# Kernel tuning notes

Hardware: AMD Instinct MI355X
Metric: run time of the kernel (lower is better)

The kernel has to match this reference:

```python
import jax, jax.numpy as jnp
import numpy as np

NOISE = 0.02
P_CONST = 1.0
NUM_LAYERS = 7


def setup_inputs() -> dict:
    key = jax.random.key(0)
    k1, k2, k3, k4 = jax.random.split(key, 4)
    B, Nt, K, L = 2048, 64, 40, NUM_LAYERS
    sqrtP = np.sqrt(P_CONST)
    return {
        'H_real': jax.random.normal(k1, (B, Nt, K), dtype=jnp.float32),
        'H_imag': jax.random.normal(k2, (B, Nt, K), dtype=jnp.float32),
        'eta': jnp.ones((L,), dtype=jnp.float32) * (0.1 / sqrtP),
        'U': jax.random.normal(k3, (L, Nt, Nt), dtype=jnp.float32) * (0.01 / sqrtP),
        'b': jax.random.normal(k4, (L, Nt, K), dtype=jnp.float32) * (0.01 / sqrtP),
    }


def _rate_total(Wr, Wi, Hc):
    # sum over batch of (sum_k log2(1+sinr_k) - power_penalty)
    W = Wr + 1j * Wi                                   # [B,Nt,K] complex
    HW = jnp.einsum('bnk,bnl->bkl', jnp.conj(Hc), W)   # [B,K,K]
    pw = jnp.abs(HW) ** 2                              # |h_k^H w_l|^2
    desired = jnp.diagonal(pw, axis1=1, axis2=2)       # [B,K]
    interference = pw.sum(axis=2) - desired
    sinr = desired / (interference + NOISE)
    rates = jnp.log2(1.0 + sinr).sum()
    power = jnp.sum(Wr * Wr + Wi * Wi, axis=(1, 2))    # ||W||_F^2 per batch
    penalty = jnp.mean((power - P_CONST) ** 2) * 0.01
    B = Wr.shape[0]
    return rates - B * penalty


def reference(H_real, H_imag, eta, U, b):
    Hc = H_real + 1j * H_imag
    B, Nt, K = H_real.shape
    Wr = jnp.zeros((B, Nt, K), dtype=jnp.float32)
    Wi = jnp.zeros((B, Nt, K), dtype=jnp.float32)
    grad_fn = jax.grad(_rate_total, argnums=(0, 1))
    for t in range(NUM_LAYERS):
        g_r, g_i = grad_fn(Wr, Wi, Hc)                 # torch grad: dL/dx + i dL/dy
        Ug_r = jnp.einsum('nm,bmk->bnk', U[t], g_r)
        Ug_i = jnp.einsum('nm,bmk->bnk', U[t], g_i)
        step_r = Ug_r - Ug_i
        step_i = Ug_i + Ug_r
        Wr = Wr - eta[t] * step_r + b[t]
        Wi = Wi - eta[t] * step_i
    # final power normalization
    norm = jnp.sqrt(jnp.sum(Wr * Wr + Wi * Wi, axis=(1, 2), keepdims=True))
    scale = jnp.sqrt(P_CONST) / (norm + 1e-6)
    Wr = Wr * scale
    Wi = Wi * scale
    return Wr + 1j * Wi
```

## Files before the change

kernel.cpp:

```cpp
#include <hip/hip_runtime.h>
#include <math.h>

typedef _Float16 h16;
typedef __attribute__((ext_vector_type(2))) _Float16 h16x2;
typedef __attribute__((ext_vector_type(4))) _Float16 h16x4;
typedef __attribute__((ext_vector_type(8))) _Float16 h16x8;
typedef __attribute__((ext_vector_type(4))) float f32x4;

#define NBATCH 2048
#define NT 64
#define KK 40
#define NL 7
#define SIGMA 0.02f
#define INVLN2 1.4426950408889634f

#define RA   0
#define RB   (40*128)
#define HCK  (2*40*128)
#define UOF  (3*40*128)
#define LDSH (UOF + 64*64)

#define SWZ(row, c)  ((c) ^ (((row)&7)<<3))
#define SWZW(row, c) ((c) ^ (((row)&15)<<3))
#define MFMA16(a,b,c) __builtin_amdgcn_mfma_f32_16x16x32_f16((a),(b),(c),0,0,0)

static __device__ __forceinline__ float DOT2(h16x2 a, h16x2 b, float c) {
#if __has_builtin(__builtin_amdgcn_fdot2)
    return __builtin_amdgcn_fdot2(a, b, c, false);
#else
    return fmaf((float)a.x, (float)b.x, fmaf((float)a.y, (float)b.y, c));
#endif
}
static __device__ __forceinline__ h16x2 PK(float x, float y) {
    h16x2 r; r.x = (h16)x; r.y = (h16)y; return r;
}
static __device__ __forceinline__ h16x8 conjA(h16x8 v) {
    union { h16x8 h; unsigned u[4]; } x; x.h = v;
    #pragma unroll
    for (int i=0;i<4;++i){ unsigned t=x.u[i]; t=(t>>16)|(t<<16); x.u[i]=t^0x80000000u; }
    return x.h;
}
static __device__ __forceinline__ h16x8 imB(h16x8 v) {
    union { h16x8 h; unsigned u[4]; } x; x.h = v;
    #pragma unroll
    for (int i=0;i<4;++i){ unsigned t=x.u[i]; t=(t>>16)|(t<<16); x.u[i]=t^0x00008000u; }
    return x.h;
}
static __device__ __forceinline__ h16x8 zsel(h16x8 v, bool p) {
    union { h16x8 h; unsigned u[4]; } x; x.h = v;
    #pragma unroll
    for (int i=0;i<4;++i) x.u[i] = p ? x.u[i] : 0u;
    return x.h;
}

__global__ __launch_bounds__(256, 2) void gpnet_kernel(
    const float* __restrict__ gHr, const float* __restrict__ gHi,
    const float* __restrict__ gEta, const float* __restrict__ gU,
    const float* __restrict__ gB, float* __restrict__ gOut, int outFloats)
{
    __shared__ __align__(16) h16 sh[LDSH];
    __shared__ float sRed[4];

    const int tid = threadIdx.x;
    const int wv  = tid >> 6;
    const int ln  = tid & 63;
    const int col = ln & 15;
    const int g   = ln >> 4;

    const int bb = blockIdx.x;
    const float* hr = gHr + (size_t)bb * NT * KK;
    const float* hi = gHi + (size_t)bb * NT * KK;

    for (int i = tid; i < NT*KK; i += 256) {
        int n = i / KK, k = i % KK;
        *(h16x2*)(sh + HCK + k*128 + SWZW(k, 2*n)) = PK(hr[i], hi[i]);
        *(h16x2*)(sh + RA  + k*128 + SWZW(k, 2*n)) = PK(gB[i], 0.f);
    }
    float Wr[3][4], Wi[3][4];
    float ps = 0.f;
    #pragma unroll
    for (int ct = 0; ct < 3; ++ct)
        #pragma unroll
        for (int r = 0; r < 4; ++r) {
            int n = 16*wv + 4*g + r, l = col + 16*ct;
            float b0 = (l < KK) ? gB[n*KK + l] : 0.f;
            Wr[ct][r] = b0; Wi[ct][r] = 0.f;
            ps += b0 * b0;
        }
    #pragma unroll
    for (int off = 32; off; off >>= 1) ps += __shfl_down(ps, off, 64);
    if (ln == 0) sRed[wv] = ps;
    __syncthreads();

    for (int t = 1; t < NL; ++t) {
        const int P = (t & 1) ? RA : RB;
        const int Q = (t & 1) ? RB : RA;
        const int GREo = P, GIMo = P + 40*64;

        const float pw   = sRed[0] + sRed[1] + sRed[2] + sRed[3];
        const float cpen = 0.04f * (pw - 1.0f);
        const float etat = gEta[t];

        if (wv < 3) {
            const int kcol = col + 16*wv;
            const bool vK = (kcol < KK);
            const int kC = vK ? kcol : 0;
            #pragma unroll
            for (int rt = 0; rt < 3; ++rt) {
                f32x4 aRe = (f32x4){0.f,0.f,0.f,0.f};
                f32x4 aIm = (f32x4){0.f,0.f,0.f,0.f};
                const int lrow = col + 16*rt;
                const int lC = (lrow < KK) ? lrow : 0;
                #pragma unroll
                for (int q = 0; q < 4; ++q) {
                    h16x8 bf = *(const h16x8*)(sh + HCK + kC*128 + SWZW(kC, g*8 + 32*q));
                    bf = zsel(bf, vK);
                    h16x8 af = *(const h16x8*)(sh + P + lC*128 + SWZW(lC, g*8 + 32*q));
                    aRe = MFMA16(af, bf, aRe);
                    aIm = MFMA16(conjA(af), bf, aIm);
                }
                #pragma unroll
                for (int r = 0; r < 4; ++r) {
                    int l = 16*rt + 4*g + r;
                    if (l < KK)
                        *(h16x2*)(sh + Q + l*128 + SWZ(l, 2*kcol)) = PK(aRe[r], aIm[r]);
                }
            }
        } else {
            const float2* u2 = (const float2*)(gU + (size_t)t * NT * NT);
            #pragma unroll 8
            for (int j = 0; j < 32; ++j) {
                int e2 = j*64 + ln;
                float2 v = u2[e2];
                int n = e2 >> 5, m2 = (e2 & 31) * 2;
                *(h16x2*)(sh + UOF + n*64 + SWZ(n, m2)) = PK(v.x, v.y);
            }
        }
        __syncthreads();

        if (tid < 160) {
            const int k = tid >> 2, q = tid & 3;
            h16x2 va[10];
            #pragma unroll
            for (int ii = 0; ii < 10; ++ii)
                va[ii] = *(const h16x2*)(sh + Q + (q*10+ii)*128 + SWZ(q*10+ii, 2*k));
            float rs = 0.f, dd = 0.f;
            #pragma unroll
            for (int ii = 0; ii < 10; ++ii) rs = DOT2(va[ii], va[ii], rs);
            const int dk = k - q*10;
            if (dk >= 0 && dk < 10) dd = DOT2(va[dk], va[dk], 0.f);
            rs += __shfl_xor(rs, 1, 64); rs += __shfl_xor(rs, 2, 64);
            dd += __shfl_xor(dd, 1, 64); dd += __shfl_xor(dd, 2, 64);
            float T  = rs + SIGMA, Is = rs - dd + SIGMA;
            float cA_ = 2.f * INVLN2 / T;
            float cC_ = -2.f * INVLN2 * dd / (Is * T);
            #pragma unroll
            for (int ii = 0; ii < 10; ++ii) {
                int l = q*10 + ii;
                float c = (l == k) ? cA_ : cC_;
                *(h16x2*)(sh + Q + l*128 + SWZ(l, 2*k)) =
                    PK((float)va[ii].x * c, -(float)va[ii].y * c);
            }
        }
        __syncthreads();

        {
            const int nrow = col + 16*wv;
            const int n0w = 16*wv + 4*g;
            #pragma unroll
            for (int ct = 0; ct < 3; ++ct) {
                f32x4 gRe = (f32x4){0.f,0.f,0.f,0.f};
                f32x4 gIm = (f32x4){0.f,0.f,0.f,0.f};
                const int lr = col + 16*ct;
                const int lrC = (lr < KK) ? lr : 0;
                #pragma unroll
                for (int q = 0; q < 3; ++q) {
                    h16x8 af;
                    #pragma unroll
                    for (int j = 0; j < 8; ++j) af[j] = (h16)0.f;
                    if (q < 2 || g < 2) {
                        const int kb = g*4 + 16*q;
                        #pragma unroll
                        for (int i = 0; i < 4; ++i) {
                            h16x2 p = *(const h16x2*)(sh + HCK + (kb+i)*128 + SWZW(kb+i, 2*nrow));
                            af[2*i] = p.x; af[2*i+1] = p.y;
                        }
                    }
                    h16x8 bf = *(const h16x8*)(sh + Q + lrC*128 + SWZ(lrC, g*8 + 32*q));
                    gRe = MFMA16(af, bf, gRe);
                    gIm = MFMA16(af, imB(bf), gIm);
                }
                if (lr < KK) {
                    h16x4 g4, q4;
                    #pragma unroll
                    for (int r = 0; r < 4; ++r) {
                        g4[r] = (h16)(gRe[r] - cpen * Wr[ct][r]);
                        q4[r] = (h16)(gIm[r] - cpen * Wi[ct][r]);
                    }
                    *(h16x4*)(sh + GREo + lr*64 + SWZ(lr, n0w)) = g4;
                    *(h16x4*)(sh + GIMo + lr*64 + SWZ(lr, n0w)) = q4;
                }
            }
        }
        __syncthreads();

        float ps2 = 0.f;
        {
            const int nrow = col + 16*wv;
            const int n0w = 16*wv + 4*g;
            const float* bt = gB + (size_t)t*NT*KK;
            #pragma unroll
            for (int ct = 0; ct < 3; ++ct) {
                f32x4 cRe = (f32x4){0.f,0.f,0.f,0.f};
                f32x4 cIm = (f32x4){0.f,0.f,0.f,0.f};
                const int l = col + 16*ct;
                const int lC = (l < KK) ? l : 0;
                #pragma unroll
                for (int q = 0; q < 2; ++q) {
                    h16x8 af = *(const h16x8*)(sh + UOF + nrow*64 + SWZ(nrow, g*8 + 32*q));
                    h16x8 fre = *(const h16x8*)(sh + GREo + lC*64 + SWZ(lC, g*8 + 32*q));
                    h16x8 fim = *(const h16x8*)(sh + GIMo + lC*64 + SWZ(lC, g*8 + 32*q));
                    cRe = MFMA16(af, fre, cRe);
                    cIm = MFMA16(af, fim, cIm);
                }
                h16x8 wvv;
                #pragma unroll
                for (int r = 0; r < 4; ++r) {
                    int n = n0w + r;
                    float br = (l < KK) ? bt[n*KK + l] : 0.f;
                    float ur = cRe[r], ui = cIm[r];
                    float wr = Wr[ct][r] - etat*(ur - ui) + br;
                    float wi = Wi[ct][r] - etat*(ui + ur);
                    Wr[ct][r] = wr; Wi[ct][r] = wi;
                    wvv[2*r]   = (h16)wr;
                    wvv[2*r+1] = (h16)wi;
                    if (l < KK) ps2 += wr*wr + wi*wi;
                }
                if (t < NL-1 && l < KK)
                    *(h16x8*)(sh + Q + l*128 + SWZW(l, 2*n0w)) = wvv;
            }
        }
        #pragma unroll
        for (int off = 32; off; off >>= 1) ps2 += __shfl_down(ps2, off, 64);
        if (ln == 0) sRed[wv] = ps2;
        __syncthreads();
    }

    const float pwf   = sRed[0] + sRed[1] + sRed[2] + sRed[3];
    const float scale = 1.0f / (sqrtf(pwf) + 1e-6f);

    if (outFloats >= 2 * NBATCH * NT * KK) {
        float2* ob = (float2*)(gOut + (size_t)bb * NT * KK * 2);
        #pragma unroll
        for (int ct = 0; ct < 3; ++ct)
            #pragma unroll
            for (int r = 0; r < 4; ++r) {
                int n = 16*wv + 4*g + r, l = col + 16*ct;
                if (l < KK) {
                    float2 v; v.x = Wr[ct][r]*scale; v.y = Wi[ct][r]*scale;
                    ob[n*KK + l] = v;
                }
            }
    } else {
        float* ob = gOut + (size_t)bb * NT * KK;
        #pragma unroll
        for (int ct = 0; ct < 3; ++ct)
            #pragma unroll
            for (int r = 0; r < 4; ++r) {
                int n = 16*wv + 4*g + r, l = col + 16*ct;
                if (l < KK) ob[n*KK + l] = Wr[ct][r] * scale;
            }
    }
}

extern "C" void kernel_launch(void* const* d_in, const int* in_sizes, int n_in,
                              void* d_out, int out_size, void* d_ws, size_t ws_size,
                              hipStream_t stream) {
    (void)in_sizes; (void)n_in; (void)d_ws; (void)ws_size;
    const float* Hr  = (const float*)d_in[0];
    const float* Hi  = (const float*)d_in[1];
    const float* eta = (const float*)d_in[2];
    const float* U   = (const float*)d_in[3];
    const float* b   = (const float*)d_in[4];
    float* out = (float*)d_out;
    gpnet_kernel<<<NBATCH, 256, 0, stream>>>(Hr, Hi, eta, U, b, out, out_size);
}
```

Measured before the change: 122.9 us.

## Process one batch item per wavefront, keeping W in registers without block syncs

Each wavefront now handles a whole batch item, with four items per block, in its own LDS region. This replaces the four-wave cooperative split and removes the __syncthreads barriers in favour of wave-local compiler fences. W is held in registers as packed fp16 MFMA operands rather than fp32 and written back to LDS. U is now read straight from global memory into registers instead of being staged in LDS. The risks are lower parallelism per item (2048 waves total), higher register pressure, and fp16 storage of W between layers, which costs accuracy.

```diff
diff --git a/kernel.cpp b/kernel.cpp
--- a/kernel.cpp
+++ b/kernel.cpp
@@ -14,15 +14,17 @@
 #define SIGMA 0.02f
 #define INVLN2 1.4426950408889634f
 
-#define RA   0
-#define RB   (40*128)
-#define HCK  (2*40*128)
-#define UOF  (3*40*128)
-#define LDSH (UOF + 64*64)
+#define ITEMSZ 15360
+#define SOFF   0
+#define GREOFF 5120
+#define GIMOFF 7680
+#define HCKOFF 10240
+#define LDSH   (4*ITEMSZ)
 
 #define SWZ(row, c)  ((c) ^ (((row)&7)<<3))
 #define SWZW(row, c) ((c) ^ (((row)&15)<<3))
 #define MFMA16(a,b,c) __builtin_amdgcn_mfma_f32_16x16x32_f16((a),(b),(c),0,0,0)
+#define CFENCE() asm volatile("" ::: "memory")
 
 static __device__ __forceinline__ float DOT2(h16x2 a, h16x2 b, float c) {
 #if __has_builtin(__builtin_amdgcn_fdot2)
@@ -52,223 +54,252 @@
     for (int i=0;i<4;++i) x.u[i] = p ? x.u[i] : 0u;
     return x.h;
 }
-
-__global__ __launch_bounds__(256, 2) void gpnet_kernel(
+static __device__ __forceinline__ h16x8 zero8() {
+    h16x8 v;
+    #pragma unroll
+    for (int j=0;j<8;++j) v[j] = (h16)0.f;
+    return v;
+}
+
+__global__ __launch_bounds__(256) void gpnet_kernel(
     const float* __restrict__ gHr, const float* __restrict__ gHi,
     const float* __restrict__ gEta, const float* __restrict__ gU,
     const float* __restrict__ gB, float* __restrict__ gOut, int outFloats)
 {
     __shared__ __align__(16) h16 sh[LDSH];
-    __shared__ float sRed[4];
 
     const int tid = threadIdx.x;
     const int wv  = tid >> 6;
     const int ln  = tid & 63;
     const int col = ln & 15;
     const int g   = ln >> 4;
-
-    const int bb = blockIdx.x;
+    const int IB  = wv * ITEMSZ;
+
+    const int bb = blockIdx.x * 4 + wv;
     const float* hr = gHr + (size_t)bb * NT * KK;
     const float* hi = gHi + (size_t)bb * NT * KK;
 
-    for (int i = tid; i < NT*KK; i += 256) {
+    for (int j = 0; j < 40; ++j) {
+        int i = j*64 + ln;
         int n = i / KK, k = i % KK;
-        *(h16x2*)(sh + HCK + k*128 + SWZW(k, 2*n)) = PK(hr[i], hi[i]);
-        *(h16x2*)(sh + RA  + k*128 + SWZW(k, 2*n)) = PK(gB[i], 0.f);
+        *(h16x2*)(sh + IB + HCKOFF + k*128 + SWZW(k, 2*n)) = PK(hr[i], hi[i]);
     }
-    float Wr[3][4], Wi[3][4];
+    h16x8 Wh[4][3];
     float ps = 0.f;
     #pragma unroll
-    for (int ct = 0; ct < 3; ++ct)
-        #pragma unroll
-        for (int r = 0; r < 4; ++r) {
-            int n = 16*wv + 4*g + r, l = col + 16*ct;
-            float b0 = (l < KK) ? gB[n*KK + l] : 0.f;
-            Wr[ct][r] = b0; Wi[ct][r] = 0.f;
-            ps += b0 * b0;
+    for (int nb = 0; nb < 4; ++nb)
+        #pragma unroll
+        for (int lt = 0; lt < 3; ++lt) {
+            int l = col + 16*lt;
+            h16x8 v = zero8();
+            if (l < KK) {
+                #pragma unroll
+                for (int r = 0; r < 4; ++r) {
+                    int n = 16*nb + 4*g + r;
+                    float b0 = gB[n*KK + l];
+                    v[2*r] = (h16)b0;
+                    ps += b0 * b0;
+                }
+            }
+            Wh[nb][lt] = v;
         }
     #pragma unroll
     for (int off = 32; off; off >>= 1) ps += __shfl_down(ps, off, 64);
-    if (ln == 0) sRed[wv] = ps;
-    __syncthreads();
-
+    float pw = __shfl(ps, 0, 64);
+    CFENCE();
+
+    #pragma unroll 1
     for (int t = 1; t < NL; ++t) {
-        const int P = (t & 1) ? RA : RB;
-        const int Q = (t & 1) ? RB : RA;
-        const int GREo = P, GIMo = P + 40*64;
-
-        const float pw   = sRed[0] + sRed[1] + sRed[2] + sRed[3];
         const float cpen = 0.04f * (pw - 1.0f);
         const float etat = gEta[t];
 
-        if (wv < 3) {
-            const int kcol = col + 16*wv;
+        #pragma unroll
+        for (int kc = 0; kc < 3; ++kc) {
+            const int kcol = col + 16*kc;
             const bool vK = (kcol < KK);
             const int kC = vK ? kcol : 0;
+            h16x8 bf[4];
+            #pragma unroll
+            for (int q = 0; q < 4; ++q) {
+                bf[q] = *(const h16x8*)(sh + IB + HCKOFF + kC*128 + SWZW(kC, g*8 + 32*q));
+                bf[q] = zsel(bf[q], vK);
+            }
             #pragma unroll
             for (int rt = 0; rt < 3; ++rt) {
                 f32x4 aRe = (f32x4){0.f,0.f,0.f,0.f};
                 f32x4 aIm = (f32x4){0.f,0.f,0.f,0.f};
-                const int lrow = col + 16*rt;
-                const int lC = (lrow < KK) ? lrow : 0;
                 #pragma unroll
                 for (int q = 0; q < 4; ++q) {
-                    h16x8 bf = *(const h16x8*)(sh + HCK + kC*128 + SWZW(kC, g*8 + 32*q));
-                    bf = zsel(bf, vK);
-                    h16x8 af = *(const h16x8*)(sh + P + lC*128 + SWZW(lC, g*8 + 32*q));
-                    aRe = MFMA16(af, bf, aRe);
-                    aIm = MFMA16(conjA(af), bf, aIm);
+                    h16x8 af = Wh[q][rt];
+                    aRe = MFMA16(af, bf[q], aRe);
+                    aIm = MFMA16(conjA(af), bf[q], aIm);
                 }
                 #pragma unroll
                 for (int r = 0; r < 4; ++r) {
                     int l = 16*rt + 4*g + r;
                     if (l < KK)
-                        *(h16x2*)(sh + Q + l*128 + SWZ(l, 2*kcol)) = PK(aRe[r], aIm[r]);
-                }
-            }
-        } else {
-            const float2* u2 = (const float2*)(gU + (size_t)t * NT * NT);
-            #pragma unroll 8
-            for (int j = 0; j < 32; ++j) {
-                int e2 = j*64 + ln;
-                float2 v = u2[e2];
-                int n = e2 >> 5, m2 = (e2 & 31) * 2;
-                *(h16x2*)(sh + UOF + n*64 + SWZ(n, m2)) = PK(v.x, v.y);
-            }
-        }
-        __syncthreads();
-
-        if (tid < 160) {
-            const int k = tid >> 2, q = tid & 3;
-            h16x2 va[10];
-            #pragma unroll
-            for (int ii = 0; ii < 10; ++ii)
-                va[ii] = *(const h16x2*)(sh + Q + (q*10+ii)*128 + SWZ(q*10+ii, 2*k));
+                        *(h16x2*)(sh + IB + SOFF + l*128 + SWZ(l, 2*kcol)) =
+                            PK(aRe[r], aIm[r]);
+                }
+            }
+        }
+        CFENCE();
+
+        if (ln < KK) {
+            const int k = ln;
             float rs = 0.f, dd = 0.f;
             #pragma unroll
-            for (int ii = 0; ii < 10; ++ii) rs = DOT2(va[ii], va[ii], rs);
-            const int dk = k - q*10;
-            if (dk >= 0 && dk < 10) dd = DOT2(va[dk], va[dk], 0.f);
-            rs += __shfl_xor(rs, 1, 64); rs += __shfl_xor(rs, 2, 64);
-            dd += __shfl_xor(dd, 1, 64); dd += __shfl_xor(dd, 2, 64);
+            for (int l = 0; l < KK; ++l) {
+                h16x2 v = *(const h16x2*)(sh + IB + SOFF + l*128 + SWZ(l, 2*k));
+                float p2 = DOT2(v, v, 0.f);
+                rs += p2;
+                if (l == k) dd = p2;
+            }
             float T  = rs + SIGMA, Is = rs - dd + SIGMA;
             float cA_ = 2.f * INVLN2 / T;
             float cC_ = -2.f * INVLN2 * dd / (Is * T);
             #pragma unroll
-            for (int ii = 0; ii < 10; ++ii) {
-                int l = q*10 + ii;
+            for (int l = 0; l < KK; ++l) {
+                h16x2 v = *(const h16x2*)(sh + IB + SOFF + l*128 + SWZ(l, 2*k));
                 float c = (l == k) ? cA_ : cC_;
-                *(h16x2*)(sh + Q + l*128 + SWZ(l, 2*k)) =
-                    PK((float)va[ii].x * c, -(float)va[ii].y * c);
-            }
-        }
-        __syncthreads();
-
-        {
-            const int nrow = col + 16*wv;
-            const int n0w = 16*wv + 4*g;
-            #pragma unroll
-            for (int ct = 0; ct < 3; ++ct) {
+                *(h16x2*)(sh + IB + SOFF + l*128 + SWZ(l, 2*k)) =
+                    PK((float)v.x * c, -(float)v.y * c);
+            }
+        }
+        CFENCE();
+
+        #pragma unroll
+        for (int nb = 0; nb < 4; ++nb) {
+            const int nrow = col + 16*nb;
+            h16x8 afh[3];
+            #pragma unroll
+            for (int q = 0; q < 3; ++q) {
+                h16x8 v = zero8();
+                if (q < 2 || g < 2) {
+                    const int kb = g*4 + 16*q;
+                    #pragma unroll
+                    for (int i = 0; i < 4; ++i) {
+                        h16x2 p = *(const h16x2*)(sh + IB + HCKOFF + (kb+i)*128 + SWZW(kb+i, 2*nrow));
+                        v[2*i] = p.x; v[2*i+1] = p.y;
+                    }
+                }
+                afh[q] = v;
+            }
+            #pragma unroll
+            for (int lt = 0; lt < 3; ++lt) {
+                const int lr = col + 16*lt;
+                const int lrC = (lr < KK) ? lr : 0;
                 f32x4 gRe = (f32x4){0.f,0.f,0.f,0.f};
                 f32x4 gIm = (f32x4){0.f,0.f,0.f,0.f};
-                const int lr = col + 16*ct;
-                const int lrC = (lr < KK) ? lr : 0;
                 #pragma unroll
                 for (int q = 0; q < 3; ++q) {
-                    h16x8 af;
-                    #pragma unroll
-                    for (int j = 0; j < 8; ++j) af[j] = (h16)0.f;
-                    if (q < 2 || g < 2) {
-                        const int kb = g*4 + 16*q;
-                        #pragma unroll
-                        for (int i = 0; i < 4; ++i) {
-                            h16x2 p = *(const h16x2*)(sh + HCK + (kb+i)*128 + SWZW(kb+i, 2*nrow));
-                            af[2*i] = p.x; af[2*i+1] = p.y;
-                        }
-                    }
-                    h16x8 bf = *(const h16x8*)(sh + Q + lrC*128 + SWZ(lrC, g*8 + 32*q));
-                    gRe = MFMA16(af, bf, gRe);
-                    gIm = MFMA16(af, imB(bf), gIm);
+                    h16x8 bf = *(const h16x8*)(sh + IB + SOFF + lrC*128 + SWZ(lrC, g*8 + 32*q));
+                    gRe = MFMA16(afh[q], bf, gRe);
+                    gIm = MFMA16(afh[q], imB(bf), gIm);
                 }
                 if (lr < KK) {
                     h16x4 g4, q4;
                     #pragma unroll
                     for (int r = 0; r < 4; ++r) {
-                        g4[r] = (h16)(gRe[r] - cpen * Wr[ct][r]);
-                        q4[r] = (h16)(gIm[r] - cpen * Wi[ct][r]);
-                    }
-                    *(h16x4*)(sh + GREo + lr*64 + SWZ(lr, n0w)) = g4;
-                    *(h16x4*)(sh + GIMo + lr*64 + SWZ(lr, n0w)) = q4;
-                }
-            }
-        }
-        __syncthreads();
-
-        float ps2 = 0.f;
+                        g4[r] = (h16)(gRe[r] - cpen * (float)Wh[nb][lt][2*r]);
+                        q4[r] = (h16)(gIm[r] - cpen * (float)Wh[nb][lt][2*r+1]);
+                    }
+                    *(h16x4*)(sh + IB + GREOFF + lr*64 + SWZ(lr, 16*nb + 4*g)) = g4;
+                    *(h16x4*)(sh + IB + GIMOFF + lr*64 + SWZ(lr, 16*nb + 4*g)) = q4;
+                }
+            }
+        }
+        CFENCE();
+
+        float psn = 0.f;
         {
-            const int nrow = col + 16*wv;
-            const int n0w = 16*wv + 4*g;
-            const float* bt = gB + (size_t)t*NT*KK;
-            #pragma unroll
-            for (int ct = 0; ct < 3; ++ct) {
-                f32x4 cRe = (f32x4){0.f,0.f,0.f,0.f};
-                f32x4 cIm = (f32x4){0.f,0.f,0.f,0.f};
-                const int l = col + 16*ct;
-                const int lC = (l < KK) ? l : 0;
+            const float* ut = gU + (size_t)t * NT * NT;
+            const float* bt = gB + (size_t)t * NT * KK;
+            #pragma unroll
+            for (int nb = 0; nb < 4; ++nb) {
+                const int nrow = col + 16*nb;
+                h16x8 au[2];
                 #pragma unroll
                 for (int q = 0; q < 2; ++q) {
-                    h16x8 af = *(const h16x8*)(sh + UOF + nrow*64 + SWZ(nrow, g*8 + 32*q));
-                    h16x8 fre = *(const h16x8*)(sh + GREo + lC*64 + SWZ(lC, g*8 + 32*q));
-                    h16x8 fim = *(const h16x8*)(sh + GIMo + lC*64 + SWZ(lC, g*8 + 32*q));
-                    cRe = MFMA16(af, fre, cRe);
-                    cIm = MFMA16(af, fim, cIm);
-                }
-                h16x8 wvv;
-                #pragma unroll
-                for (int r = 0; r < 4; ++r) {
-                    int n = n0w + r;
-                    float br = (l < KK) ? bt[n*KK + l] : 0.f;
-                    float ur = cRe[r], ui = cIm[r];
-                    float wr = Wr[ct][r] - etat*(ur - ui) + br;
-                    float wi = Wi[ct][r] - etat*(ui + ur);
-                    Wr[ct][r] = wr; Wi[ct][r] = wi;
-                    wvv[2*r]   = (h16)wr;
-                    wvv[2*r+1] = (h16)wi;
-                    if (l < KK) ps2 += wr*wr + wi*wi;
-                }
-                if (t < NL-1 && l < KK)
-                    *(h16x8*)(sh + Q + l*128 + SWZW(l, 2*n0w)) = wvv;
-            }
-        }
-        #pragma unroll
-        for (int off = 32; off; off >>= 1) ps2 += __shfl_down(ps2, off, 64);
-        if (ln == 0) sRed[wv] = ps2;
-        __syncthreads();
+                    const int mb = g*8 + 32*q;
+                    float4 a = *(const float4*)(ut + nrow*64 + mb);
+                    float4 b2 = *(const float4*)(ut + nrow*64 + mb + 4);
+                    h16x8 v;
+                    v[0]=(h16)a.x; v[1]=(h16)a.y; v[2]=(h16)a.z; v[3]=(h16)a.w;
+                    v[4]=(h16)b2.x; v[5]=(h16)b2.y; v[6]=(h16)b2.z; v[7]=(h16)b2.w;
+                    au[q] = v;
+                }
+                #pragma unroll
+                for (int lt = 0; lt < 3; ++lt) {
+                    const int l = col + 16*lt;
+                    const int lC = (l < KK) ? l : 0;
+                    f32x4 cRe = (f32x4){0.f,0.f,0.f,0.f};
+                    f32x4 cIm = (f32x4){0.f,0.f,0.f,0.f};
+                    #pragma unroll
+                    for (int q = 0; q < 2; ++q) {
+                        h16x8 fre = *(const h16x8*)(sh + IB + GREOFF + lC*64 + SWZ(lC, g*8 + 32*q));
+                        h16x8 fim = *(const h16x8*)(sh + IB + GIMOFF + lC*64 + SWZ(lC, g*8 + 32*q));
+                        cRe = MFMA16(au[q], fre, cRe);
+                        cIm = MFMA16(au[q], fim, cIm);
+                    }
+                    h16x8 wnew = zero8();
+                    if (l < KK) {
+                        #pragma unroll
+                        for (int r = 0; r < 4; ++r) {
+                            int n = 16*nb + 4*g + r;
+                            float br = bt[n*KK + l];
+                            float ur = cRe[r], ui = cIm[r];
+                            float wr = (float)Wh[nb][lt][2*r]   - etat*(ur - ui) + br;
+                            float wi = (float)Wh[nb][lt][2*r+1] - etat*(ui + ur);
+                            wnew[2*r]   = (h16)wr;
+                            wnew[2*r+1] = (h16)wi;
+                            psn += wr*wr + wi*wi;
+                        }
+                    }
+                    Wh[nb][lt] = wnew;
+                }
+            }
+        }
+        #pragma unroll
+        for (int off = 32; off; off >>= 1) psn += __shfl_down(psn, off, 64);
+        pw = __shfl(psn, 0, 64);
+        CFENCE();
     }
 
-    const float pwf   = sRed[0] + sRed[1] + sRed[2] + sRed[3];
-    const float scale = 1.0f / (sqrtf(pwf) + 1e-6f);
+    const float scale = 1.0f / (sqrtf(pw) + 1e-6f);
 
     if (outFloats >= 2 * NBATCH * NT * KK) {
         float2* ob = (float2*)(gOut + (size_t)bb * NT * KK * 2);
         #pragma unroll
-        for (int ct = 0; ct < 3; ++ct)
-            #pragma unroll
-            for (int r = 0; r < 4; ++r) {
-                int n = 16*wv + 4*g + r, l = col + 16*ct;
+        for (int nb = 0; nb < 4; ++nb)
+            #pragma unroll
+            for (int lt = 0; lt < 3; ++lt) {
+                int l = col + 16*lt;
                 if (l < KK) {
-                    float2 v; v.x = Wr[ct][r]*scale; v.y = Wi[ct][r]*scale;
-                    ob[n*KK + l] = v;
+                    #pragma unroll
+                    for (int r = 0; r < 4; ++r) {
+                        int n = 16*nb + 4*g + r;
+                        float2 v;
+                        v.x = (float)Wh[nb][lt][2*r]   * scale;
+                        v.y = (float)Wh[nb][lt][2*r+1] * scale;
+                        ob[n*KK + l] = v;
+                    }
                 }
             }
     } else {
         float* ob = gOut + (size_t)bb * NT * KK;
         #pragma unroll
-        for (int ct = 0; ct < 3; ++ct)
-            #pragma unroll
-            for (int r = 0; r < 4; ++r) {
-                int n = 16*wv + 4*g + r, l = col + 16*ct;
-                if (l < KK) ob[n*KK + l] = Wr[ct][r] * scale;
+        for (int nb = 0; nb < 4; ++nb)
+            #pragma unroll
+            for (int lt = 0; lt < 3; ++lt) {
+                int l = col + 16*lt;
+                if (l < KK) {
+                    #pragma unroll
+                    for (int r = 0; r < 4; ++r) {
+                        int n = 16*nb + 4*g + r;
+                        ob[n*KK + l] = (float)Wh[nb][lt][2*r] * scale;
+                    }
+                }
             }
     }
 }
@@ -283,5 +314,5 @@
     const float* U   = (const float*)d_in[3];
     const float* b   = (const float*)d_in[4];
     float* out = (float*)d_out;
-    gpnet_kernel<<<NBATCH, 256, 0, stream>>>(Hr, Hi, eta, U, b, out, out_size);
-}
+    gpnet_kernel<<<NBATCH/4, 256, 0, stream>>>(Hr, Hi, eta, U, b, out, out_size);
+}
```

New measurement: 127.4 us. 3.6% more time.
